# Kernel tuning notes

Hardware: AMD Instinct MI355X
Metric: run time of the kernel (lower is better)

The kernel has to match this reference:

```python
import jax, jax.numpy as jnp
import numpy as np

B, C, E = 4, 2048, 1024
H, D = 16, 64  # num_heads, head_size

def setup_inputs() -> dict:
    key = jax.random.key(0)
    kx, kk, kq, kv, ko = jax.random.split(key, 5)
    s = 1.0 / np.sqrt(E)
    so = 1.0 / np.sqrt(H * D)
    return {
        "x": jax.random.normal(kx, (B, C, E), dtype=jnp.float32),
        "Wk": jax.random.uniform(kk, (H * D, E), jnp.float32, -s, s),
        "Wq": jax.random.uniform(kq, (H * D, E), jnp.float32, -s, s),
        "Wv": jax.random.uniform(kv, (H * D, E), jnp.float32, -s, s),
        "Wo": jax.random.uniform(ko, (E, H * D), jnp.float32, -so, so),
    }

def reference(x, Wk, Wq, Wv, Wo):
    b, c, e = x.shape
    # projections -> [B, H, C, D]
    def proj(W):
        return (x @ W.T).reshape(b, c, H, D).transpose(0, 2, 1, 3)
    k = proj(Wk)
    q = proj(Wq)
    v = proj(Wv)
    # scores [B, H, C, C]; mask applied before scaling (as in source; -inf*scale = -inf)
    sa = jnp.einsum("bhqd,bhkd->bhqk", q, k)
    mask = ~jnp.tril(jnp.ones((c, c), dtype=bool))  # True above diagonal
    masked = jnp.where(mask, -jnp.inf, sa)
    scale = 1.0 / np.sqrt(D)
    attn = jax.nn.softmax(masked * scale, axis=-1)
    out = jnp.einsum("bhqk,bhkd->bhqd", attn, v)  # [B, H, C, D]
    flat = out.transpose(0, 2, 1, 3).reshape(b, c, H * D)
    return flat @ Wo.T
```

## Files before the change

kernel.cpp:

```cpp
#include <hip/hip_runtime.h>
#include <hip/hip_bf16.h>

typedef __bf16 bf16x8 __attribute__((ext_vector_type(8)));
typedef __bf16 bf16x4 __attribute__((ext_vector_type(4)));
typedef float f32x4 __attribute__((ext_vector_type(4)));

#define NEG_INF (-__builtin_inff())

__global__ void cvt_f32_bf16(const float* __restrict__ src, __bf16* __restrict__ dst, int n) {
    int idx = blockIdx.x * blockDim.x + threadIdx.x;
    int stride = gridDim.x * blockDim.x;
    for (int i = idx * 4; i < n; i += stride * 4) {
        float4 v = *(const float4*)(src + i);
        bf16x4 o;
        o[0] = (__bf16)v.x; o[1] = (__bf16)v.y; o[2] = (__bf16)v.z; o[3] = (__bf16)v.w;
        *(bf16x4*)(dst + i) = o;
    }
}

template <int MODE>
__launch_bounds__(256, 3)
__global__ void gemm_bt(const __bf16* __restrict__ A, const __bf16* __restrict__ Bm,
                        void* __restrict__ Out, int M, int N, int K) {
    __shared__ __align__(1024) char smem[32768];
    const int tid = threadIdx.x;
    const int w = tid >> 6, lane = tid & 63;
    const int lr = lane & 15, lg = lane >> 4;
    const int wm0 = (w >> 1) * 64, wn0 = (w & 1) * 64;

    const int nbx = gridDim.x;
    int id = blockIdx.y * nbx + blockIdx.x;
    int q8 = (nbx * gridDim.y) >> 3;
    int vid = (id & 7) * q8 + (id >> 3);
    const int m0 = (vid / nbx) * 128, n0 = (vid % nbx) * 128;

    const char* Ab = (const char*)A;
    const char* Bb = (const char*)Bm;

    f32x4 acc[4][4] = {};

    const int s_row_in_chunk = lane >> 3;
    const int s_col16 = lane & 7;

    const int nt = K >> 6;
    for (int t = 0; t < nt; ++t) {
#pragma unroll
        for (int r = 0; r < 4; ++r) {
            int c = w * 4 + r;
            int row = c * 8 + s_row_in_chunk;
            const char* srcA = Ab + ((size_t)(m0 + row) * K + t * 64) * 2 + s_col16 * 16;
            const char* srcB = Bb + ((size_t)(n0 + row) * K + t * 64) * 2 + s_col16 * 16;
            __builtin_amdgcn_global_load_lds(
                (const __attribute__((address_space(1))) void*)srcA,
                (__attribute__((address_space(3))) void*)(smem + c * 1024), 16, 0, 0);
            __builtin_amdgcn_global_load_lds(
                (const __attribute__((address_space(1))) void*)srcB,
                (__attribute__((address_space(3))) void*)(smem + 16384 + c * 1024), 16, 0, 0);
        }
        __syncthreads();

#pragma unroll
        for (int kk = 0; kk < 2; ++kk) {
            bf16x8 af[4], bf[4];
#pragma unroll
            for (int mi = 0; mi < 4; ++mi)
                af[mi] = *(const bf16x8*)(smem + (wm0 + mi * 16 + lr) * 128 + kk * 64 + lg * 16);
#pragma unroll
            for (int ni = 0; ni < 4; ++ni)
                bf[ni] = *(const bf16x8*)(smem + 16384 + (wn0 + ni * 16 + lr) * 128 + kk * 64 + lg * 16);
            __builtin_amdgcn_s_setprio(1);
#pragma unroll
            for (int mi = 0; mi < 4; ++mi)
#pragma unroll
                for (int ni = 0; ni < 4; ++ni)
                    acc[mi][ni] = __builtin_amdgcn_mfma_f32_16x16x32_bf16(
                        af[mi], bf[ni], acc[mi][ni], 0, 0, 0);
            __builtin_amdgcn_s_setprio(0);
        }
        __syncthreads();
    }

#pragma unroll
    for (int mi = 0; mi < 4; ++mi)
#pragma unroll
        for (int ni = 0; ni < 4; ++ni)
#pragma unroll
            for (int r = 0; r < 4; ++r) {
                int m = m0 + wm0 + mi * 16 + lg * 4 + r;
                int n = n0 + wn0 + ni * 16 + lr;
                float v = acc[mi][ni][r];
                if (MODE == 0) {
                    int proj = n >> 10, nn = n & 1023;
                    int h = nn >> 6, d = nn & 63;
                    int bb = m >> 11, c = m & 2047;
                    if (proj == 2) {
                        ((__bf16*)Out)[(size_t)2 * 8388608 +
                                       ((size_t)((bb * 16 + h) * 64 + d)) * 2048 + c] = (__bf16)v;
                    } else {
                        float scale = (proj == 0) ? 0.125f : 1.0f;
                        ((__bf16*)Out)[(size_t)proj * 8388608 +
                                       ((size_t)(bb * 16 + h) * 2048 + c) * 64 + d] =
                            (__bf16)(v * scale);
                    }
                } else {
                    ((float*)Out)[(size_t)m * N + n] = v;
                }
            }
}

__device__ __forceinline__ unsigned swz(unsigned d) {
    return d ^ (((d >> 7) & 7) << 4);
}

__launch_bounds__(256, 4)
__global__ void attn_fwd(const __bf16* __restrict__ Q, const __bf16* __restrict__ K,
                         const __bf16* __restrict__ Vt, __bf16* __restrict__ Aout) {
    __shared__ char smem[40960];
    const int id = blockIdx.x;
    const int vid = (id & 7) * 128 + (id >> 3);
    const int bh = vid >> 4, pr = vid & 15;
    const int w = threadIdx.x >> 6, lane = threadIdx.x & 63;
    const int lr = lane & 15, lg = lane >> 4;
    const char* Kb  = (const char*)(K  + (size_t)bh * 2048 * 64);
    const char* Vtb = (const char*)(Vt + (size_t)bh * 64 * 2048);
    const __bf16* Qb = Q + (size_t)bh * 2048 * 64;
    const int b = bh >> 4, h = bh & 15;
    char* Pb = smem + 32768 + w * 2048;

    for (int pass = 0; pass < 2; ++pass) {
        const int qt = pass ? pr : 31 - pr;
        const int q0 = qt * 64 + w * 16;
        const int nt = qt + 1;

        bf16x8 qf[2];
#pragma unroll
        for (int kk = 0; kk < 2; ++kk)
            qf[kk] = *(const bf16x8*)&Qb[(size_t)(q0 + lr) * 64 + kk * 32 + lg * 8];

        f32x4 o[4] = {};
        float m = NEG_INF, l = 0.f;

        __syncthreads();
        {
            char* kd = smem;
            char* vd = smem + 16384;
#pragma unroll
            for (int i = 0; i < 2; ++i) {
                unsigned c = (unsigned)(w * 2 + i);
                unsigned d = c * 1024 + (unsigned)lane * 16;
                unsigned bs = swz(d);
                __builtin_amdgcn_global_load_lds(
                    (const __attribute__((address_space(1))) void*)(Kb + bs),
                    (__attribute__((address_space(3))) void*)(kd + c * 1024), 16, 0, 0);
                unsigned row = bs >> 7, colb = bs & 127;
                __builtin_amdgcn_global_load_lds(
                    (const __attribute__((address_space(1))) void*)(Vtb + (size_t)row * 4096 + colb),
                    (__attribute__((address_space(3))) void*)(vd + c * 1024), 16, 0, 0);
            }
        }

        for (int t = 0; t < nt; ++t) {
            __syncthreads();
            if (t + 1 < nt) {
                char* kd = smem + ((t + 1) & 1) * 8192;
                char* vd = smem + 16384 + ((t + 1) & 1) * 8192;
#pragma unroll
                for (int i = 0; i < 2; ++i) {
                    unsigned c = (unsigned)(w * 2 + i);
                    unsigned d = c * 1024 + (unsigned)lane * 16;
                    unsigned bs = swz(d);
                    __builtin_amdgcn_global_load_lds(
                        (const __attribute__((address_space(1))) void*)(Kb + (size_t)(t + 1) * 8192 + bs),
                        (__attribute__((address_space(3))) void*)(kd + c * 1024), 16, 0, 0);
                    unsigned row = bs >> 7, colb = bs & 127;
                    __builtin_amdgcn_global_load_lds(
                        (const __attribute__((address_space(1))) void*)(Vtb + (size_t)row * 4096 +
                                                                       (size_t)(t + 1) * 128 + colb),
                        (__attribute__((address_space(3))) void*)(vd + c * 1024), 16, 0, 0);
                }
            }
            const char* Ks = smem + (t & 1) * 8192;
            const char* Vs = smem + 16384 + (t & 1) * 8192;
            const int k0 = t * 64;

            f32x4 s[4] = {};
#pragma unroll
            for (int kk = 0; kk < 2; ++kk)
#pragma unroll
                for (int sub = 0; sub < 4; ++sub) {
                    bf16x8 kf = *(const bf16x8*)(Ks + swz((unsigned)((sub * 16 + lr) * 128 + kk * 64 + lg * 16)));
                    s[sub] = __builtin_amdgcn_mfma_f32_16x16x32_bf16(kf, qf[kk], s[sub], 0, 0, 0);
                }
            if (t == qt) {
#pragma unroll
                for (int sub = 0; sub < 4; ++sub)
#pragma unroll
                    for (int r = 0; r < 4; ++r)
                        if (k0 + sub * 16 + lg * 4 + r > q0 + lr) s[sub][r] = NEG_INF;
            }
            float mloc = NEG_INF;
#pragma unroll
            for (int sub = 0; sub < 4; ++sub)
#pragma unroll
                for (int r = 0; r < 4; ++r) mloc = fmaxf(mloc, s[sub][r]);
            mloc = fmaxf(mloc, __shfl_xor(mloc, 16));
            mloc = fmaxf(mloc, __shfl_xor(mloc, 32));
            float mnew = fmaxf(m, mloc);
            float alpha = __expf(m - mnew);
            float rs = 0.f;
#pragma unroll
            for (int sub = 0; sub < 4; ++sub)
#pragma unroll
                for (int r = 0; r < 4; ++r) {
                    float p = __expf(s[sub][r] - mnew);
                    s[sub][r] = p;
                    rs += p;
                }
            rs += __shfl_xor(rs, 16);
            rs += __shfl_xor(rs, 32);
            l = l * alpha + rs;
            m = mnew;
#pragma unroll
            for (int ni = 0; ni < 4; ++ni) o[ni] *= alpha;

#pragma unroll
            for (int sub = 0; sub < 4; ++sub) {
                bf16x4 pk;
#pragma unroll
                for (int r = 0; r < 4; ++r) pk[r] = (__bf16)s[sub][r];
                *(bf16x4*)(Pb + swz((unsigned)(lr * 128 + sub * 32 + lg * 8))) = pk;
            }
            bf16x8 pfr[2];
#pragma unroll
            for (int kk = 0; kk < 2; ++kk)
                pfr[kk] = *(const bf16x8*)(Pb + swz((unsigned)(lr * 128 + kk * 64 + lg * 16)));

#pragma unroll
            for (int kk = 0; kk < 2; ++kk)
#pragma unroll
                for (int ni = 0; ni < 4; ++ni) {
                    bf16x8 vf = *(const bf16x8*)(Vs + swz((unsigned)((ni * 16 + lr) * 128 + kk * 64 + lg * 16)));
                    o[ni] = __builtin_amdgcn_mfma_f32_16x16x32_bf16(vf, pfr[kk], o[ni], 0, 0, 0);
                }
        }

        float rinv = 1.0f / l;
#pragma unroll
        for (int ni = 0; ni < 4; ++ni) {
            bf16x4 ov;
#pragma unroll
            for (int r = 0; r < 4; ++r) ov[r] = (__bf16)(o[ni][r] * rinv);
            *(bf16x4*)&Aout[((size_t)b * 2048 + q0 + lr) * 1024 + h * 64 + ni * 16 + lg * 4] = ov;
        }
    }
}

extern "C" void kernel_launch(void* const* d_in, const int* in_sizes, int n_in,
                              void* d_out, int out_size, void* d_ws, size_t ws_size,
                              hipStream_t stream) {
    const float* x  = (const float*)d_in[0];
    const float* Wk = (const float*)d_in[1];
    const float* Wq = (const float*)d_in[2];
    const float* Wv = (const float*)d_in[3];
    const float* Wo = (const float*)d_in[4];

    char* ws = (char*)d_ws;
    __bf16* xb   = (__bf16*)(ws);
    __bf16* wqkv = (__bf16*)(ws + 16777216);
    __bf16* wo_b = (__bf16*)(ws + 23068672);
    __bf16* qkv  = (__bf16*)(ws + 25165824);
    __bf16* aout = (__bf16*)(ws + 75497472);
    float* out = (float*)d_out;

    cvt_f32_bf16<<<2048, 256, 0, stream>>>(x, xb, 8388608);
    cvt_f32_bf16<<<1024, 256, 0, stream>>>(Wq, wqkv, 1048576);
    cvt_f32_bf16<<<1024, 256, 0, stream>>>(Wk, wqkv + 1048576, 1048576);
    cvt_f32_bf16<<<1024, 256, 0, stream>>>(Wv, wqkv + 2097152, 1048576);
    cvt_f32_bf16<<<1024, 256, 0, stream>>>(Wo, wo_b, 1048576);

    gemm_bt<0><<<dim3(24, 64), 256, 0, stream>>>(xb, wqkv, qkv, 8192, 3072, 1024);
    attn_fwd<<<dim3(1024), 256, 0, stream>>>(qkv, qkv + 8388608, qkv + 16777216, aout);
    gemm_bt<1><<<dim3(8, 64), 256, 0, stream>>>(aout, wo_b, out, 8192, 1024, 1024);
}
```

Before: 192.0 us.

## Share K/V tiles between paired query tiles and fuse conversion kernels

The attention kernel now processes both paired query tiles (31-pr and pr) in one sweep over the key range, so each K/V tile loaded into LDS serves both tiles for the overlapping prefix instead of being reloaded in a second pass. This roughly halves K/V global traffic and barrier count per block, at the cost of doubled accumulator and Q-fragment registers, which may pressure occupancy under launch_bounds(256,4). Separately, the five f32-to-bf16 conversion launches are merged into one kernel to cut launch overhead.

```diff
diff --git a/kernel.cpp b/kernel.cpp
--- a/kernel.cpp
+++ b/kernel.cpp
@@ -7,15 +7,28 @@
 
 #define NEG_INF (-__builtin_inff())
 
-__global__ void cvt_f32_bf16(const float* __restrict__ src, __bf16* __restrict__ dst, int n) {
-    int idx = blockIdx.x * blockDim.x + threadIdx.x;
-    int stride = gridDim.x * blockDim.x;
-    for (int i = idx * 4; i < n; i += stride * 4) {
-        float4 v = *(const float4*)(src + i);
-        bf16x4 o;
-        o[0] = (__bf16)v.x; o[1] = (__bf16)v.y; o[2] = (__bf16)v.z; o[3] = (__bf16)v.w;
-        *(bf16x4*)(dst + i) = o;
-    }
+__global__ void cvt_all(const float* __restrict__ x,
+                        const float* __restrict__ Wq, const float* __restrict__ Wk,
+                        const float* __restrict__ Wv, const float* __restrict__ Wo,
+                        __bf16* __restrict__ xb, __bf16* __restrict__ wqkv,
+                        __bf16* __restrict__ wo_b) {
+    int i = (blockIdx.x * blockDim.x + threadIdx.x) * 4;
+    const float* src;
+    __bf16* dst;
+    int off;
+    if (i < 8388608) {
+        src = x; dst = xb; off = i;
+    } else {
+        int j = i - 8388608;
+        int sel = j >> 20;
+        off = j & 1048575;
+        src = (sel == 0) ? Wq : (sel == 1) ? Wk : (sel == 2) ? Wv : Wo;
+        dst = (sel < 3) ? (wqkv + (size_t)sel * 1048576) : wo_b;
+    }
+    float4 v = *(const float4*)(src + off);
+    bf16x4 o;
+    o[0] = (__bf16)v.x; o[1] = (__bf16)v.y; o[2] = (__bf16)v.z; o[3] = (__bf16)v.w;
+    *(bf16x4*)(dst + off) = o;
 }
 
 template <int MODE>
@@ -39,7 +52,7 @@
 
     f32x4 acc[4][4] = {};
 
-    const int s_row_in_chunk = lane >> 3;
+    const int s_row8 = lane >> 3;
     const int s_col16 = lane & 7;
 
     const int nt = K >> 6;
@@ -47,7 +60,7 @@
 #pragma unroll
         for (int r = 0; r < 4; ++r) {
             int c = w * 4 + r;
-            int row = c * 8 + s_row_in_chunk;
+            int row = c * 8 + s_row8;
             const char* srcA = Ab + ((size_t)(m0 + row) * K + t * 64) * 2 + s_col16 * 16;
             const char* srcB = Bb + ((size_t)(n0 + row) * K + t * 64) * 2 + s_col16 * 16;
             __builtin_amdgcn_global_load_lds(
@@ -127,62 +140,64 @@
     const int b = bh >> 4, h = bh & 15;
     char* Pb = smem + 32768 + w * 2048;
 
-    for (int pass = 0; pass < 2; ++pass) {
-        const int qt = pass ? pr : 31 - pr;
-        const int q0 = qt * 64 + w * 16;
-        const int nt = qt + 1;
-
-        bf16x8 qf[2];
-#pragma unroll
-        for (int kk = 0; kk < 2; ++kk)
-            qf[kk] = *(const bf16x8*)&Qb[(size_t)(q0 + lr) * 64 + kk * 32 + lg * 8];
-
-        f32x4 o[4] = {};
-        float m = NEG_INF, l = 0.f;
-
+    const int qta = 31 - pr, qtb = pr;
+    const int q0a = qta * 64 + w * 16, q0b = qtb * 64 + w * 16;
+
+    bf16x8 qfa[2], qfb[2];
+#pragma unroll
+    for (int kk = 0; kk < 2; ++kk) {
+        qfa[kk] = *(const bf16x8*)&Qb[(size_t)(q0a + lr) * 64 + kk * 32 + lg * 8];
+        qfb[kk] = *(const bf16x8*)&Qb[(size_t)(q0b + lr) * 64 + kk * 32 + lg * 8];
+    }
+
+    f32x4 oa[4] = {}, ob[4] = {};
+    float ma = NEG_INF, la = 0.f, mb = NEG_INF, lb = 0.f;
+
+    {
+        char* kd = smem;
+        char* vd = smem + 16384;
+#pragma unroll
+        for (int i = 0; i < 2; ++i) {
+            unsigned c = (unsigned)(w * 2 + i);
+            unsigned d = c * 1024 + (unsigned)lane * 16;
+            unsigned bs = swz(d);
+            __builtin_amdgcn_global_load_lds(
+                (const __attribute__((address_space(1))) void*)(Kb + bs),
+                (__attribute__((address_space(3))) void*)(kd + c * 1024), 16, 0, 0);
+            unsigned row = bs >> 7, colb = bs & 127;
+            __builtin_amdgcn_global_load_lds(
+                (const __attribute__((address_space(1))) void*)(Vtb + (size_t)row * 4096 + colb),
+                (__attribute__((address_space(3))) void*)(vd + c * 1024), 16, 0, 0);
+        }
+    }
+
+    const int nt = qta + 1;
+    for (int t = 0; t < nt; ++t) {
         __syncthreads();
-        {
-            char* kd = smem;
-            char* vd = smem + 16384;
+        if (t + 1 < nt) {
+            char* kd = smem + ((t + 1) & 1) * 8192;
+            char* vd = smem + 16384 + ((t + 1) & 1) * 8192;
 #pragma unroll
             for (int i = 0; i < 2; ++i) {
                 unsigned c = (unsigned)(w * 2 + i);
                 unsigned d = c * 1024 + (unsigned)lane * 16;
                 unsigned bs = swz(d);
                 __builtin_amdgcn_global_load_lds(
-                    (const __attribute__((address_space(1))) void*)(Kb + bs),
+                    (const __attribute__((address_space(1))) void*)(Kb + (size_t)(t + 1) * 8192 + bs),
                     (__attribute__((address_space(3))) void*)(kd + c * 1024), 16, 0, 0);
                 unsigned row = bs >> 7, colb = bs & 127;
                 __builtin_amdgcn_global_load_lds(
-                    (const __attribute__((address_space(1))) void*)(Vtb + (size_t)row * 4096 + colb),
+                    (const __attribute__((address_space(1))) void*)(Vtb + (size_t)row * 4096 +
+                                                                   (size_t)(t + 1) * 128 + colb),
                     (__attribute__((address_space(3))) void*)(vd + c * 1024), 16, 0, 0);
             }
         }
-
-        for (int t = 0; t < nt; ++t) {
-            __syncthreads();
-            if (t + 1 < nt) {
-                char* kd = smem + ((t + 1) & 1) * 8192;
-                char* vd = smem + 16384 + ((t + 1) & 1) * 8192;
-#pragma unroll
-                for (int i = 0; i < 2; ++i) {
-                    unsigned c = (unsigned)(w * 2 + i);
-                    unsigned d = c * 1024 + (unsigned)lane * 16;
-                    unsigned bs = swz(d);
-                    __builtin_amdgcn_global_load_lds(
-                        (const __attribute__((address_space(1))) void*)(Kb + (size_t)(t + 1) * 8192 + bs),
-                        (__attribute__((address_space(3))) void*)(kd + c * 1024), 16, 0, 0);
-                    unsigned row = bs >> 7, colb = bs & 127;
-                    __builtin_amdgcn_global_load_lds(
-                        (const __attribute__((address_space(1))) void*)(Vtb + (size_t)row * 4096 +
-                                                                       (size_t)(t + 1) * 128 + colb),
-                        (__attribute__((address_space(3))) void*)(vd + c * 1024), 16, 0, 0);
-                }
-            }
-            const char* Ks = smem + (t & 1) * 8192;
-            const char* Vs = smem + 16384 + (t & 1) * 8192;
-            const int k0 = t * 64;
-
+        const char* Ks = smem + (t & 1) * 8192;
+        const char* Vs = smem + 16384 + (t & 1) * 8192;
+        const int k0 = t * 64;
+
+        auto process = [&](const bf16x8 (&qf)[2], int q0, bool diag,
+                           f32x4 (&o)[4], float& m, float& l) {
             f32x4 s[4] = {};
 #pragma unroll
             for (int kk = 0; kk < 2; ++kk)
@@ -191,7 +206,7 @@
                     bf16x8 kf = *(const bf16x8*)(Ks + swz((unsigned)((sub * 16 + lr) * 128 + kk * 64 + lg * 16)));
                     s[sub] = __builtin_amdgcn_mfma_f32_16x16x32_bf16(kf, qf[kk], s[sub], 0, 0, 0);
                 }
-            if (t == qt) {
+            if (diag) {
 #pragma unroll
                 for (int sub = 0; sub < 4; ++sub)
 #pragma unroll
@@ -242,16 +257,23 @@
                     bf16x8 vf = *(const bf16x8*)(Vs + swz((unsigned)((ni * 16 + lr) * 128 + kk * 64 + lg * 16)));
                     o[ni] = __builtin_amdgcn_mfma_f32_16x16x32_bf16(vf, pfr[kk], o[ni], 0, 0, 0);
                 }
-        }
-
-        float rinv = 1.0f / l;
-#pragma unroll
-        for (int ni = 0; ni < 4; ++ni) {
-            bf16x4 ov;
-#pragma unroll
-            for (int r = 0; r < 4; ++r) ov[r] = (__bf16)(o[ni][r] * rinv);
-            *(bf16x4*)&Aout[((size_t)b * 2048 + q0 + lr) * 1024 + h * 64 + ni * 16 + lg * 4] = ov;
-        }
+        };
+
+        process(qfa, q0a, t == qta, oa, ma, la);
+        if (t <= qtb) process(qfb, q0b, t == qtb, ob, mb, lb);
+    }
+
+    float ra = 1.0f / la, rb = 1.0f / lb;
+#pragma unroll
+    for (int ni = 0; ni < 4; ++ni) {
+        bf16x4 va, vb;
+#pragma unroll
+        for (int r = 0; r < 4; ++r) {
+            va[r] = (__bf16)(oa[ni][r] * ra);
+            vb[r] = (__bf16)(ob[ni][r] * rb);
+        }
+        *(bf16x4*)&Aout[((size_t)b * 2048 + q0a + lr) * 1024 + h * 64 + ni * 16 + lg * 4] = va;
+        *(bf16x4*)&Aout[((size_t)b * 2048 + q0b + lr) * 1024 + h * 64 + ni * 16 + lg * 4] = vb;
     }
 }
 
@@ -272,11 +294,7 @@
     __bf16* aout = (__bf16*)(ws + 75497472);
     float* out = (float*)d_out;
 
-    cvt_f32_bf16<<<2048, 256, 0, stream>>>(x, xb, 8388608);
-    cvt_f32_bf16<<<1024, 256, 0, stream>>>(Wq, wqkv, 1048576);
-    cvt_f32_bf16<<<1024, 256, 0, stream>>>(Wk, wqkv + 1048576, 1048576);
-    cvt_f32_bf16<<<1024, 256, 0, stream>>>(Wv, wqkv + 2097152, 1048576);
-    cvt_f32_bf16<<<1024, 256, 0, stream>>>(Wo, wo_b, 1048576);
+    cvt_all<<<12288, 256, 0, stream>>>(x, Wq, Wk, Wv, Wo, xb, wqkv, wo_b);
 
     gemm_bt<0><<<dim3(24, 64), 256, 0, stream>>>(xb, wqkv, qkv, 8192, 3072, 1024);
     attn_fwd<<<dim3(1024), 256, 0, stream>>>(qkv, qkv + 8388608, qkv + 16777216, aout);
```

New measurement: 187.5 us (median of 3 runs). -2.3%, faster.
